# Kernel tuning notes

Measured on AMD Instinct MI355X. Metric: run time of the kernel, lower is better.

## Reference

```python
import jax, jax.numpy as jnp
import numpy as np
import math

B, S, D = 4, 2048, 768
H = 12
DH = D // H  # 64
NEG = -1e10

def setup_inputs() -> dict:
    key = jax.random.key(0)
    ks = jax.random.split(key, 8)
    scale = 0.02
    return {
        "hidden_states": jax.random.normal(ks[0], (B, S, D), dtype=jnp.float32),
        "attention_mask": jnp.zeros((B, 1, 1, S), dtype=jnp.float32),
        "Wq": jax.random.normal(ks[1], (D, D), dtype=jnp.float32) * scale,
        "bq": jnp.zeros((D,), dtype=jnp.float32),
        "Wk": jax.random.normal(ks[2], (D, D), dtype=jnp.float32) * scale,
        "bk": jnp.zeros((D,), dtype=jnp.float32),
        "Wv": jax.random.normal(ks[3], (D, D), dtype=jnp.float32) * scale,
        "bv": jnp.zeros((D,), dtype=jnp.float32),
    }

def reference(hidden_states, attention_mask, Wq, bq, Wk, bk, Wv, bv):
    # Linear projections; note attention_mask is accepted but unused, matching the torch module.
    def split_heads(x):  # [B,S,D] -> [B,H,S,DH]
        return x.reshape(B, S, H, DH).transpose(0, 2, 1, 3)
    q = split_heads(hidden_states @ Wq + bq)
    k = split_heads(hidden_states @ Wk + bk)
    v = split_heads(hidden_states @ Wv + bv)
    scores = jnp.einsum("bhqd,bhkd->bhqk", q, k) / math.sqrt(DH)
    causal = jnp.tril(jnp.ones((S, S), dtype=bool))  # masked_fill(mask==0, -1e10)
    scores = jnp.where(causal, scores, NEG)
    probs = jax.nn.softmax(scores, axis=-1)
    # dropout prob = 0.0 (eval) -> identity
    ctx = jnp.einsum("bhqk,bhkd->bhqd", probs, v)
    return ctx.transpose(0, 2, 1, 3).reshape(B, S, D)
```

## Files before the change

### kernel.cpp

```cpp
#include <hip/hip_runtime.h>
#include <hip/hip_bf16.h>

#define B_  4
#define S_  2048
#define D_  768
#define H_  12
#define DH_ 64

typedef __bf16 bf16;
typedef __attribute__((ext_vector_type(8))) __bf16 bf16x8;
typedef __attribute__((ext_vector_type(4))) __bf16 bf16x4;
typedef __attribute__((ext_vector_type(4))) float floatx4;
typedef __attribute__((ext_vector_type(4))) short short4v;

#if defined(__has_builtin)
#if __has_builtin(__builtin_amdgcn_mfma_f32_16x16x16bf16_1k)
#define HAVE_MFMA16_BUILTIN 1
#endif
#endif
static __device__ __forceinline__ floatx4 mfma16(short4v a, short4v b, floatx4 c) {
#ifdef HAVE_MFMA16_BUILTIN
    return __builtin_amdgcn_mfma_f32_16x16x16bf16_1k(a, b, c, 0, 0, 0);
#else
    floatx4 d = c;
    asm("v_mfma_f32_16x16x16_bf16 %0, %1, %2, %0" : "+v"(d) : "v"(a), "v"(b));
    return d;
#endif
}

__device__ __forceinline__ int swz(int row, int col) {
    return row * 64 + (col ^ ((row & 7) << 3));
}

__device__ __forceinline__ void gload16(const bf16* g, bf16* l) {
    __builtin_amdgcn_global_load_lds(
        (const __attribute__((address_space(1))) void*)g,
        (__attribute__((address_space(3))) void*)l, 16, 0, 0);
}

__device__ __forceinline__ int chunk_off(int qt) {
    if (qt < 8)  return qt;
    if (qt < 16) return 8 + 2 * (qt - 8);
    if (qt < 24) return 24 + 3 * (qt - 16);
    return 48 + 4 * (qt - 24);
}

__global__ __launch_bounds__(256) void prep(const float* __restrict__ hs,
                                            const float* __restrict__ w0,
                                            const float* __restrict__ w1,
                                            const float* __restrict__ w2,
                                            bf16* __restrict__ Xb,
                                            bf16* __restrict__ Wt)
{
    __shared__ bf16 t[64 * 72];
    const int bid = blockIdx.x;
    const int tid = threadIdx.x;
    if (bid < 6144) {
        int i = bid * 256 + tid;
        float4 v = ((const float4*)hs)[i];
        bf16x4 o;
        o[0] = (bf16)v.x; o[1] = (bf16)v.y; o[2] = (bf16)v.z; o[3] = (bf16)v.w;
        *(bf16x4*)(Xb + (size_t)i * 4) = o;
        return;
    }
    const int t4 = bid - 6144;
    const int which = t4 / 144;
    const int rem = t4 % 144;
    const float* W = (which == 0) ? w0 : (which == 1 ? w1 : w2);
    bf16* dst = Wt + (size_t)which * D_ * D_;
    const int k0 = (rem / 12) * 64, n0 = (rem % 12) * 64;
    {
        int r = tid >> 2;
        int c0 = (tid & 3) * 16;
        #pragma unroll
        for (int q = 0; q < 4; q++) {
            float4 v = *(const float4*)(W + (size_t)(k0 + r) * D_ + n0 + c0 + q * 4);
            t[(c0 + q * 4 + 0) * 72 + r] = (bf16)v.x;
            t[(c0 + q * 4 + 1) * 72 + r] = (bf16)v.y;
            t[(c0 + q * 4 + 2) * 72 + r] = (bf16)v.z;
            t[(c0 + q * 4 + 3) * 72 + r] = (bf16)v.w;
        }
    }
    __syncthreads();
    {
        int n = tid >> 3, seg = tid & 7;
        *(bf16x8*)(dst + (size_t)(n0 + n) * D_ + k0 + seg * 8) =
            *(const bf16x8*)(t + n * 72 + seg * 8);
        *(bf16x8*)(dst + (size_t)(n0 + n + 32) * D_ + k0 + seg * 8) =
            *(const bf16x8*)(t + (n + 32) * 72 + seg * 8);
    }
}

__global__ __launch_bounds__(256) void qkv_gemm(
    const bf16* __restrict__ Xb, const bf16* __restrict__ Wt,
    const float* __restrict__ bq, const float* __restrict__ bk,
    const float* __restrict__ bv, bf16* __restrict__ QKV)
{
    const int which = blockIdx.z;
    const bf16* Wm = Wt + (size_t)which * D_ * D_;
    const float* bias = (which == 0) ? bq : (which == 1 ? bk : bv);
    bf16* out = QKV + (size_t)which * B_ * H_ * S_ * DH_;

    __shared__ bf16 As[128 * 64];
    __shared__ bf16 Bs[128 * 64];

    const int tid  = threadIdx.x;
    const int wave = tid >> 6, lane = tid & 63;
    const int wr = wave >> 1, wc = wave & 1;
    const int g = lane >> 4, ln = lane & 15;
    const int m0 = blockIdx.x * 128, n0 = blockIdx.y * 128;

    floatx4 acc[4][4];
    #pragma unroll
    for (int i = 0; i < 4; i++)
        #pragma unroll
        for (int j = 0; j < 4; j++)
            acc[i][j] = (floatx4){0.f, 0.f, 0.f, 0.f};

    int row_[4], scol_[4];
    #pragma unroll
    for (int t = 0; t < 4; t++) {
        int c = tid + t * 256;
        row_[t]  = c >> 3;
        scol_[t] = ((c & 7) * 8) ^ ((row_[t] & 7) << 3);
    }

    for (int k0 = 0; k0 < D_; k0 += 64) {
        if (k0) __syncthreads();
        #pragma unroll
        for (int t = 0; t < 4; t++) {
            bf16* ldst = As + (size_t)(t * 256 + wave * 64) * 8;
            gload16(Xb + (size_t)(m0 + row_[t]) * D_ + k0 + scol_[t], ldst);
        }
        #pragma unroll
        for (int t = 0; t < 4; t++) {
            bf16* ldst = Bs + (size_t)(t * 256 + wave * 64) * 8;
            gload16(Wm + (size_t)(n0 + row_[t]) * D_ + k0 + scol_[t], ldst);
        }
        __syncthreads();
        #pragma unroll
        for (int ks = 0; ks < 2; ks++) {
            bf16x8 af[4], bfr[4];
            #pragma unroll
            for (int i = 0; i < 4; i++)
                af[i] = *(const bf16x8*)(As + swz(wr * 64 + i * 16 + ln, ks * 32 + g * 8));
            #pragma unroll
            for (int j = 0; j < 4; j++)
                bfr[j] = *(const bf16x8*)(Bs + swz(wc * 64 + j * 16 + ln, ks * 32 + g * 8));
            #pragma unroll
            for (int i = 0; i < 4; i++)
                #pragma unroll
                for (int j = 0; j < 4; j++)
                    acc[i][j] = __builtin_amdgcn_mfma_f32_16x16x32_bf16(af[i], bfr[j], acc[i][j], 0, 0, 0);
        }
    }

    #pragma unroll
    for (int i = 0; i < 4; i++) {
        #pragma unroll
        for (int j = 0; j < 4; j++) {
            int col = n0 + wc * 64 + j * 16 + ln;
            float bv_ = bias[col];
            int h = col >> 6, dh = col & 63;
            int rowbase = m0 + wr * 64 + i * 16 + g * 4;
            int b = rowbase >> 11, s0 = rowbase & 2047;
            if (which == 2) {
                bf16x4 o;
                #pragma unroll
                for (int r = 0; r < 4; r++) o[r] = (bf16)(acc[i][j][r] + bv_);
                *(bf16x4*)(out + ((size_t)((b * H_ + h) * DH_ + dh)) * S_ + s0) = o;
            } else {
                #pragma unroll
                for (int r = 0; r < 4; r++)
                    out[(((size_t)(b * H_ + h) * S_ + s0 + r) << 6) + dh] =
                        (bf16)(acc[i][j][r] + bv_);
            }
        }
    }
}

__global__ __launch_bounds__(256, 4) void attn_chunk(const bf16* __restrict__ QKV,
                                                     float* __restrict__ out,
                                                     bf16* __restrict__ Opart,
                                                     float* __restrict__ Lpart)
{
    const int cid = 79 - blockIdx.x;
    const int bh = blockIdx.y;
    const int b = bh / H_, h = bh % H_;

    int qt, c;
    if (cid < 8)       { qt = cid; c = 0; }
    else if (cid < 24) { qt = 8 + ((cid - 8) >> 1); c = (cid - 8) & 1; }
    else if (cid < 48) { int t3 = cid - 24; qt = 16 + t3 / 3; c = t3 - (qt - 16) * 3; }
    else               { int t4 = cid - 48; qt = 24 + (t4 >> 2); c = t4 & 3; }
    const int nch = (qt >> 3) + 1;
    const int kt0 = c * 8;
    const int kt1 = min(kt0 + 7, qt);

    const size_t MAT = (size_t)B_ * H_ * S_ * DH_;
    const bf16* Q  = QKV +           (size_t)bh * S_ * DH_;
    const bf16* K  = QKV + MAT +     (size_t)bh * S_ * DH_;
    const bf16* Vt = QKV + 2 * MAT + (size_t)bh * S_ * DH_;

    __shared__ bf16 Ks[64 * 64];
    __shared__ bf16 Vts[64 * 64];

    const int tid  = threadIdx.x;
    const int wave = tid >> 6, lane = tid & 63;
    const int g = lane >> 4, ln = lane & 15;
    const int srow = tid >> 3, sseg = tid & 7;

    bf16x8 qf[2];
    {
        const bf16* qrow = Q + (size_t)(qt * 64 + wave * 16 + ln) * DH_;
        qf[0] = *(const bf16x8*)(qrow + g * 8);
        qf[1] = *(const bf16x8*)(qrow + 32 + g * 8);
    }

    const short4v ones16 = {0x3F80, 0x3F80, 0x3F80, 0x3F80};

    floatx4 accO[4];
    #pragma unroll
    for (int dt = 0; dt < 4; dt++) accO[dt] = (floatx4){0.f, 0.f, 0.f, 0.f};
    floatx4 accL = (floatx4){0.f, 0.f, 0.f, 0.f};

    const bf16* kptr = K  + (size_t)(kt0 * 64 + srow) * DH_ + sseg * 8;
    const bf16* vptr = Vt + (size_t)srow * S_ + kt0 * 64 + sseg * 8;

    bf16x8 ka = *(const bf16x8*)kptr;
    bf16x8 kb = *(const bf16x8*)(kptr + 32 * DH_);
    bf16x8 va = *(const bf16x8*)vptr;
    bf16x8 vb = *(const bf16x8*)(vptr + (size_t)32 * S_);

    for (int kt = kt0; kt <= kt1; ++kt) {
        __syncthreads();
        *(bf16x8*)(Ks  + swz(srow, sseg * 8)) = ka;
        *(bf16x8*)(Ks  + swz(srow + 32, sseg * 8)) = kb;
        *(bf16x8*)(Vts + swz(srow, sseg * 8)) = va;
        *(bf16x8*)(Vts + swz(srow + 32, sseg * 8)) = vb;
        __syncthreads();
        if (kt < kt1) {
            kptr += 64 * DH_;
            vptr += 64;
            ka = *(const bf16x8*)kptr;
            kb = *(const bf16x8*)(kptr + 32 * DH_);
            va = *(const bf16x8*)vptr;
            vb = *(const bf16x8*)(vptr + (size_t)32 * S_);
        }

        __builtin_amdgcn_s_setprio(1);
        #pragma unroll
        for (int j = 0; j < 4; j++) {
            floatx4 accS = (floatx4){0.f, 0.f, 0.f, 0.f};
            #pragma unroll
            for (int cc = 0; cc < 2; cc++) {
                bf16x8 kf = *(const bf16x8*)(Ks + swz(j * 16 + ln, cc * 32 + g * 8));
                accS = __builtin_amdgcn_mfma_f32_16x16x32_bf16(kf, qf[cc], accS, 0, 0, 0);
            }

            #pragma unroll
            for (int r = 0; r < 4; r++) accS[r] = __expf(accS[r] * 0.125f);
            if (kt == qt) {
                const int krow = j * 16 + g * 4;
                const int qrow = wave * 16 + ln;
                #pragma unroll
                for (int r = 0; r < 4; r++)
                    if (krow + r > qrow) accS[r] = 0.f;
            }

            bf16x4 pa;
            #pragma unroll
            for (int r = 0; r < 4; r++) pa[r] = (bf16)accS[r];
            short4v pas = __builtin_bit_cast(short4v, pa);

            accL = mfma16(pas, ones16, accL);

            #pragma unroll
            for (int dt = 0; dt < 4; dt++) {
                short4v vf = *(const short4v*)(Vts + swz(dt * 16 + ln, j * 16 + g * 4));
                accO[dt] = mfma16(pas, vf, accO[dt]);
            }
        }
        __builtin_amdgcn_s_setprio(0);
    }

    if (nch == 1) {
        float inv[4];
        #pragma unroll
        for (int r = 0; r < 4; r++) inv[r] = 1.0f / accL[r];
        #pragma unroll
        for (int dt = 0; dt < 4; dt++) {
            int dh = dt * 16 + ln;
            #pragma unroll
            for (int r = 0; r < 4; r++) {
                int q = qt * 64 + wave * 16 + g * 4 + r;
                out[((size_t)(b * S_ + q)) * D_ + h * DH_ + dh] = accO[dt][r] * inv[r];
            }
        }
    } else {
        const int chunk = bh * 80 + chunk_off(qt) + c;
        bf16x8 p0, p1;
        #pragma unroll
        for (int e = 0; e < 8; e++) {
            p0[e] = (bf16)accO[e >> 2][e & 3];
            p1[e] = (bf16)accO[2 + (e >> 2)][e & 3];
        }
        bf16* dst = Opart + (size_t)chunk * 4096 + tid * 16;
        *(bf16x8*)dst = p0;
        *(bf16x8*)(dst + 8) = p1;
        if (ln == 0) {
            #pragma unroll
            for (int r = 0; r < 4; r++)
                Lpart[chunk * 64 + wave * 16 + g * 4 + r] = accL[r];
        }
    }
}

__global__ __launch_bounds__(256) void attn_reduce(const bf16* __restrict__ Opart,
                                                   const float* __restrict__ Lpart,
                                                   float* __restrict__ out)
{
    const int qt = 8 + blockIdx.x;
    const int bh = blockIdx.y;
    const int b = bh / H_, h = bh % H_;
    const int nch = (qt >> 3) + 1;
    const int cb = bh * 80 + chunk_off(qt);

    const int tid  = threadIdx.x;
    const int wave = tid >> 6, lane = tid & 63;
    const int g = lane >> 4, ln = lane & 15;

    float o[16];
    #pragma unroll
    for (int e = 0; e < 16; e++) o[e] = 0.f;
    float ls[4] = {0.f, 0.f, 0.f, 0.f};

    for (int cidx = 0; cidx < nch; cidx++) {
        const bf16* p = Opart + (size_t)(cb + cidx) * 4096 + tid * 16;
        bf16x8 v0 = *(const bf16x8*)p;
        bf16x8 v1 = *(const bf16x8*)(p + 8);
        #pragma unroll
        for (int e = 0; e < 8; e++) { o[e] += (float)v0[e]; o[8 + e] += (float)v1[e]; }
        #pragma unroll
        for (int r = 0; r < 4; r++)
            ls[r] += Lpart[(cb + cidx) * 64 + wave * 16 + g * 4 + r];
    }
    float inv[4];
    #pragma unroll
    for (int r = 0; r < 4; r++) inv[r] = 1.0f / ls[r];
    #pragma unroll
    for (int j = 0; j < 4; j++) {
        int dh = j * 16 + ln;
        #pragma unroll
        for (int r = 0; r < 4; r++) {
            int q = qt * 64 + wave * 16 + g * 4 + r;
            out[((size_t)(b * S_ + q)) * D_ + h * DH_ + dh] = o[j * 4 + r] * inv[r];
        }
    }
}

extern "C" void kernel_launch(void* const* d_in, const int* in_sizes, int n_in,
                              void* d_out, int out_size, void* d_ws, size_t ws_size,
                              hipStream_t stream) {
    const float* hs = (const float*)d_in[0];
    const float* Wq = (const float*)d_in[2];
    const float* bq = (const float*)d_in[3];
    const float* Wk = (const float*)d_in[4];
    const float* bk = (const float*)d_in[5];
    const float* Wv = (const float*)d_in[6];
    const float* bv = (const float*)d_in[7];
    float* out = (float*)d_out;

    bf16* Xb    = (bf16*)d_ws;
    bf16* Wt    = Xb + (size_t)8192 * 768;
    bf16* QKV   = Wt + (size_t)3 * 768 * 768;
    bf16* Opart = QKV + (size_t)3 * B_ * H_ * S_ * DH_;
    float* Lpart = (float*)(Opart + (size_t)3840 * 4096);

    prep<<<6576, 256, 0, stream>>>(hs, Wq, Wk, Wv, Xb, Wt);
    qkv_gemm<<<dim3(64, 6, 3), 256, 0, stream>>>(Xb, Wt, bq, bk, bv, QKV);
    attn_chunk<<<dim3(80, 48), 256, 0, stream>>>(QKV, out, Opart, Lpart);
    attn_reduce<<<dim3(24, 48), 256, 0, stream>>>(Opart, Lpart, out);
}
```

Baseline: 189.9 us.

## Fold softmax scale into Q weights, use 16-tile KV chunks, split attention launch

Q weights and bias are pre-multiplied by log2(e)/sqrt(64), so the attention kernel can use a raw exp2 in place of a scaled expf. The KV split changes from chunks of 8 key tiles (up to 4 partials) to chunks of 16 (at most 2 partials). This means fewer partial writes and a simpler, fixed two-way reduce. The attention launch is split into two half-grids over batch-heads. Larger chunks give fewer, longer blocks, which may leave CUs less evenly loaded.

```diff
diff --git a/kernel.cpp b/kernel.cpp
--- a/kernel.cpp
+++ b/kernel.cpp
@@ -6,6 +6,8 @@
 #define D_  768
 #define H_  12
 #define DH_ 64
+
+#define QSCALE 0.1803368802f
 
 typedef __bf16 bf16;
 typedef __attribute__((ext_vector_type(8))) __bf16 bf16x8;
@@ -39,10 +41,7 @@
 }
 
 __device__ __forceinline__ int chunk_off(int qt) {
-    if (qt < 8)  return qt;
-    if (qt < 16) return 8 + 2 * (qt - 8);
-    if (qt < 24) return 24 + 3 * (qt - 16);
-    return 48 + 4 * (qt - 24);
+    return (qt < 16) ? qt : 16 + 2 * (qt - 16);
 }
 
 __global__ __launch_bounds__(256) void prep(const float* __restrict__ hs,
@@ -67,6 +66,7 @@
     const int which = t4 / 144;
     const int rem = t4 % 144;
     const float* W = (which == 0) ? w0 : (which == 1 ? w1 : w2);
+    const float sc = (which == 0) ? QSCALE : 1.0f;
     bf16* dst = Wt + (size_t)which * D_ * D_;
     const int k0 = (rem / 12) * 64, n0 = (rem % 12) * 64;
     {
@@ -75,10 +75,10 @@
         #pragma unroll
         for (int q = 0; q < 4; q++) {
             float4 v = *(const float4*)(W + (size_t)(k0 + r) * D_ + n0 + c0 + q * 4);
-            t[(c0 + q * 4 + 0) * 72 + r] = (bf16)v.x;
-            t[(c0 + q * 4 + 1) * 72 + r] = (bf16)v.y;
-            t[(c0 + q * 4 + 2) * 72 + r] = (bf16)v.z;
-            t[(c0 + q * 4 + 3) * 72 + r] = (bf16)v.w;
+            t[(c0 + q * 4 + 0) * 72 + r] = (bf16)(v.x * sc);
+            t[(c0 + q * 4 + 1) * 72 + r] = (bf16)(v.y * sc);
+            t[(c0 + q * 4 + 2) * 72 + r] = (bf16)(v.z * sc);
+            t[(c0 + q * 4 + 3) * 72 + r] = (bf16)(v.w * sc);
         }
     }
     __syncthreads();
@@ -99,6 +99,7 @@
     const int which = blockIdx.z;
     const bf16* Wm = Wt + (size_t)which * D_ * D_;
     const float* bias = (which == 0) ? bq : (which == 1 ? bk : bv);
+    const float bscale = (which == 0) ? QSCALE : 1.0f;
     bf16* out = QKV + (size_t)which * B_ * H_ * S_ * DH_;
 
     __shared__ bf16 As[128 * 64];
@@ -160,7 +161,7 @@
         #pragma unroll
         for (int j = 0; j < 4; j++) {
             int col = n0 + wc * 64 + j * 16 + ln;
-            float bv_ = bias[col];
+            float bv_ = bias[col] * bscale;
             int h = col >> 6, dh = col & 63;
             int rowbase = m0 + wr * 64 + i * 16 + g * 4;
             int b = rowbase >> 11, s0 = rowbase & 2047;
@@ -182,20 +183,19 @@
 __global__ __launch_bounds__(256, 4) void attn_chunk(const bf16* __restrict__ QKV,
                                                      float* __restrict__ out,
                                                      bf16* __restrict__ Opart,
-                                                     float* __restrict__ Lpart)
+                                                     float* __restrict__ Lpart,
+                                                     int bh_base)
 {
-    const int cid = 79 - blockIdx.x;
-    const int bh = blockIdx.y;
+    const int cid = 47 - blockIdx.x;
+    const int bh = bh_base + blockIdx.y;
     const int b = bh / H_, h = bh % H_;
 
     int qt, c;
-    if (cid < 8)       { qt = cid; c = 0; }
-    else if (cid < 24) { qt = 8 + ((cid - 8) >> 1); c = (cid - 8) & 1; }
-    else if (cid < 48) { int t3 = cid - 24; qt = 16 + t3 / 3; c = t3 - (qt - 16) * 3; }
-    else               { int t4 = cid - 48; qt = 24 + (t4 >> 2); c = t4 & 3; }
-    const int nch = (qt >> 3) + 1;
-    const int kt0 = c * 8;
-    const int kt1 = min(kt0 + 7, qt);
+    if (cid < 16) { qt = cid; c = 0; }
+    else          { int t = cid - 16; qt = 16 + (t >> 1); c = t & 1; }
+    const int nch = (qt >> 4) + 1;
+    const int kt0 = c * 16;
+    const int kt1 = min(kt0 + 15, qt);
 
     const size_t MAT = (size_t)B_ * H_ * S_ * DH_;
     const bf16* Q  = QKV +           (size_t)bh * S_ * DH_;
@@ -259,7 +259,7 @@
             }
 
             #pragma unroll
-            for (int r = 0; r < 4; r++) accS[r] = __expf(accS[r] * 0.125f);
+            for (int r = 0; r < 4; r++) accS[r] = __builtin_amdgcn_exp2f(accS[r]);
             if (kt == qt) {
                 const int krow = j * 16 + g * 4;
                 const int qrow = wave * 16 + ln;
@@ -298,7 +298,7 @@
             }
         }
     } else {
-        const int chunk = bh * 80 + chunk_off(qt) + c;
+        const int chunk = bh * 48 + chunk_off(qt) + c;
         bf16x8 p0, p1;
         #pragma unroll
         for (int e = 0; e < 8; e++) {
@@ -320,30 +320,34 @@
                                                    const float* __restrict__ Lpart,
                                                    float* __restrict__ out)
 {
-    const int qt = 8 + blockIdx.x;
+    const int qt = 16 + blockIdx.x;
     const int bh = blockIdx.y;
     const int b = bh / H_, h = bh % H_;
-    const int nch = (qt >> 3) + 1;
-    const int cb = bh * 80 + chunk_off(qt);
+    const int cb = bh * 48 + chunk_off(qt);
 
     const int tid  = threadIdx.x;
     const int wave = tid >> 6, lane = tid & 63;
     const int g = lane >> 4, ln = lane & 15;
 
     float o[16];
-    #pragma unroll
-    for (int e = 0; e < 16; e++) o[e] = 0.f;
-    float ls[4] = {0.f, 0.f, 0.f, 0.f};
-
-    for (int cidx = 0; cidx < nch; cidx++) {
-        const bf16* p = Opart + (size_t)(cb + cidx) * 4096 + tid * 16;
-        bf16x8 v0 = *(const bf16x8*)p;
-        bf16x8 v1 = *(const bf16x8*)(p + 8);
-        #pragma unroll
-        for (int e = 0; e < 8; e++) { o[e] += (float)v0[e]; o[8 + e] += (float)v1[e]; }
+    float ls[4];
+
+    {
+        const bf16* p0 = Opart + (size_t)cb * 4096 + tid * 16;
+        const bf16* p1 = Opart + (size_t)(cb + 1) * 4096 + tid * 16;
+        bf16x8 a0 = *(const bf16x8*)p0;
+        bf16x8 a1 = *(const bf16x8*)(p0 + 8);
+        bf16x8 b0 = *(const bf16x8*)p1;
+        bf16x8 b1 = *(const bf16x8*)(p1 + 8);
+        #pragma unroll
+        for (int e = 0; e < 8; e++) {
+            o[e]     = (float)a0[e] + (float)b0[e];
+            o[8 + e] = (float)a1[e] + (float)b1[e];
+        }
         #pragma unroll
         for (int r = 0; r < 4; r++)
-            ls[r] += Lpart[(cb + cidx) * 64 + wave * 16 + g * 4 + r];
+            ls[r] = Lpart[cb * 64 + wave * 16 + g * 4 + r] +
+                    Lpart[(cb + 1) * 64 + wave * 16 + g * 4 + r];
     }
     float inv[4];
     #pragma unroll
@@ -375,10 +379,11 @@
     bf16* Wt    = Xb + (size_t)8192 * 768;
     bf16* QKV   = Wt + (size_t)3 * 768 * 768;
     bf16* Opart = QKV + (size_t)3 * B_ * H_ * S_ * DH_;
-    float* Lpart = (float*)(Opart + (size_t)3840 * 4096);
+    float* Lpart = (float*)(Opart + (size_t)2304 * 4096);
 
     prep<<<6576, 256, 0, stream>>>(hs, Wq, Wk, Wv, Xb, Wt);
     qkv_gemm<<<dim3(64, 6, 3), 256, 0, stream>>>(Xb, Wt, bq, bk, bv, QKV);
-    attn_chunk<<<dim3(80, 48), 256, 0, stream>>>(QKV, out, Opart, Lpart);
-    attn_reduce<<<dim3(24, 48), 256, 0, stream>>>(Opart, Lpart, out);
-}
+    attn_chunk<<<dim3(48, 24), 256, 0, stream>>>(QKV, out, Opart, Lpart, 0);
+    attn_chunk<<<dim3(48, 24), 256, 0, stream>>>(QKV, out, Opart, Lpart, 24);
+    attn_reduce<<<dim3(16, 48), 256, 0, stream>>>(Opart, Lpart, out);
+}
```

Measured after the change: 204.3 us. +7.6%, slower.
